# Performance work log

Hardware: AMD Instinct MI355X
Metric: run time of the kernel (lower is better)

The kernel has to match this reference:

```python
import jax, jax.numpy as jnp
import numpy as np

B, S, D_IN, D_OUT, R = 4, 1024, 1024, 1024, 8

def setup_inputs() -> dict:
    key = jax.random.key(0)
    k1, k2, k3, k4, k5 = jax.random.split(key, 5)
    scale = 1.0 / np.sqrt(D_IN)
    return {
        "x": jax.random.normal(k1, (B, S, D_IN), dtype=jnp.float32),
        "A_params": jax.random.normal(k2, (B, S, D_OUT, R), dtype=jnp.float32) * 0.02,
        "B_params": jax.random.normal(k3, (B, S, R, D_IN), dtype=jnp.float32) * 0.02,
        "W": jax.random.normal(k4, (D_OUT, D_IN), dtype=jnp.float32) * scale,
        "b": jax.random.normal(k5, (D_OUT,), dtype=jnp.float32) * scale,
    }

def reference(x, A_params, B_params, W, b):
    # base linear: y = x @ W^T + b  -> [B, S, D_OUT]
    base_out = jnp.einsum('bsi,oi->bso', x, W) + b
    # per-token low-rank update: (x @ B^T) @ A^T
    inter = jnp.einsum('bsi,bsri->bsr', x, B_params)           # [B, S, R]
    adaptation = jnp.einsum('bsr,bsor->bso', inter, A_params)  # [B, S, D_OUT]
    return base_out + adaptation
```

## Files before the change

kernel.cpp:

```cpp
#include <hip/hip_runtime.h>
#include <hip/hip_bf16.h>
#include <stdint.h>

#define TOKENS 4096
#define DIN 1024
#define DOUT 1024
#define RANK 8
#define BM 128
#define BN 64
#define BK 64

typedef __attribute__((ext_vector_type(4))) float f32x4;
typedef __attribute__((ext_vector_type(8))) short short8;

__device__ __forceinline__ unsigned short f2bf(float f) {
    union { float f; unsigned u; } v; v.f = f;
    unsigned r = v.u + 0x7FFFu + ((v.u >> 16) & 1u);
    return (unsigned short)(r >> 16);
}

__global__ __launch_bounds__(256) void k_inter_cvt(const float* __restrict__ x,
                                                   const float* __restrict__ Bp,
                                                   const float* __restrict__ W,
                                                   float* __restrict__ inter,
                                                   ushort* __restrict__ xb,
                                                   ushort* __restrict__ Wb) {
    const int bid = blockIdx.x;
    const int tid = threadIdx.x;

    if (bid >= 1024) {
        const int b2 = bid - 1024;
        const float4* w4 = (const float4*)(W + (size_t)b2 * 4096);
        ushort4* o4 = (ushort4*)(Wb + (size_t)b2 * 4096);
#pragma unroll
        for (int j = 0; j < 4; ++j) {
            float4 v = w4[j * 256 + tid];
            ushort4 u;
            u.x = f2bf(v.x); u.y = f2bf(v.y); u.z = f2bf(v.z); u.w = f2bf(v.w);
            o4[j * 256 + tid] = u;
        }
        return;
    }

    const int lane = tid & 63, wave = tid >> 6;
    const int t = bid * 4 + wave;

    const float4* x4 = (const float4*)(x + (size_t)t * DIN);
    float4 xv[4];
#pragma unroll
    for (int j = 0; j < 4; ++j) xv[j] = x4[j * 64 + lane];

    ushort4* xb4 = (ushort4*)(xb + (size_t)t * DIN);
#pragma unroll
    for (int j = 0; j < 4; ++j) {
        ushort4 u;
        u.x = f2bf(xv[j].x); u.y = f2bf(xv[j].y);
        u.z = f2bf(xv[j].z); u.w = f2bf(xv[j].w);
        xb4[j * 64 + lane] = u;
    }

    const float4* B4 = (const float4*)(Bp + (size_t)t * RANK * DIN);
    float acc[RANK];
#pragma unroll
    for (int r = 0; r < RANK; ++r) {
        float s = 0.f;
#pragma unroll
        for (int j = 0; j < 4; ++j) {
            float4 bv = B4[r * 256 + j * 64 + lane];
            s += bv.x * xv[j].x + bv.y * xv[j].y + bv.z * xv[j].z + bv.w * xv[j].w;
        }
        acc[r] = s;
    }

#pragma unroll
    for (int r = 0; r < RANK; ++r) {
#pragma unroll
        for (int off = 32; off > 0; off >>= 1)
            acc[r] += __shfl_xor(acc[r], off, 64);
    }

    if (lane == 0) {
        float4 lo, hi;
        lo.x = acc[0]; lo.y = acc[1]; lo.z = acc[2]; lo.w = acc[3];
        hi.x = acc[4]; hi.y = acc[5]; hi.z = acc[6]; hi.w = acc[7];
        float4* ip = (float4*)(inter + (size_t)t * RANK);
        ip[0] = lo; ip[1] = hi;
    }
}

__global__ __launch_bounds__(256, 2) void k_gemm_fused(const ushort* __restrict__ Xb,
                                                       const ushort* __restrict__ Wb,
                                                       const float* __restrict__ bias,
                                                       const float* __restrict__ inter,
                                                       const float* __restrict__ Ap,
                                                       float* __restrict__ out) {
    __shared__ ushort As[2][BM * BK];
    __shared__ ushort Bs[2][BN * BK];
    __shared__ float sInter[BM * 8];
    __shared__ float sBias[BN];

    const int tid = threadIdx.x;
    const int lane = tid & 63, wave = tid >> 6;
    const int wm = wave >> 1, wn = wave & 1;

    const int bid = blockIdx.x;
    const int swz = (bid & 7) * 64 + (bid >> 3);
    const int M0 = (swz >> 4) * BM;
    const int N0 = (swz & 15) * BN;

    const int col16 = lane & 15;
    const int kg = lane >> 4;
    const int c8 = col16 & 7;

    ((float4*)sInter)[tid] = ((const float4*)(inter + (size_t)M0 * RANK))[tid];
    if (tid < 16) ((float4*)sBias)[tid] = ((const float4*)(bias + N0))[tid];

    const float* Abase = Ap + ((size_t)(M0 + wm * 64 + kg * 4) * DOUT +
                               (N0 + wn * 32 + col16)) * RANK;

    auto stage = [&](int b, int kt) {
#pragma unroll
        for (int st = 0; st < 4; ++st) {
            int flat = st * 256 + tid;
            int row = flat >> 3, ch = flat & 7;
            int chs = ch ^ (row & 7);
            const ushort* g = Xb + (size_t)(M0 + row) * DIN + kt + chs * 8;
            __builtin_amdgcn_global_load_lds(
                (const __attribute__((address_space(1))) void*)g,
                (__attribute__((address_space(3))) void*)(&As[b][flat * 8]), 16, 0, 0);
        }
#pragma unroll
        for (int st = 0; st < 2; ++st) {
            int flat = st * 256 + tid;
            int row = flat >> 3, ch = flat & 7;
            int chs = ch ^ (row & 7);
            const ushort* g = Wb + (size_t)(N0 + row) * DIN + kt + chs * 8;
            __builtin_amdgcn_global_load_lds(
                (const __attribute__((address_space(1))) void*)g,
                (__attribute__((address_space(3))) void*)(&Bs[b][flat * 8]), 16, 0, 0);
        }
    };

    auto aptr = [&](int e) {
        const int nf = e >> 3, mf = (e >> 1) & 3, rg0 = (e & 1) * 2;
        return Abase + ((size_t)(mf * 16 + rg0) * DOUT + nf * 16) * RANK;
    };

    float4 areg[2][4];

    {
        const float* Ae0 = aptr(0);
        areg[0][0] = ((const float4*)Ae0)[0];
        areg[0][1] = ((const float4*)Ae0)[1];
        areg[0][2] = ((const float4*)(Ae0 + (size_t)DOUT * RANK))[0];
        areg[0][3] = ((const float4*)(Ae0 + (size_t)DOUT * RANK))[1];
    }
    __builtin_amdgcn_sched_barrier(0);
    stage(0, 0);

    f32x4 acc[4][2] = {};

#pragma unroll
    for (int t = 0; t < 16; ++t) {
        const int cur = t & 1;

        if (t < 15) {
            const float* Ae0 = aptr(t + 1);
            areg[cur ^ 1][0] = ((const float4*)Ae0)[0];
            areg[cur ^ 1][1] = ((const float4*)Ae0)[1];
            areg[cur ^ 1][2] = ((const float4*)(Ae0 + (size_t)DOUT * RANK))[0];
            areg[cur ^ 1][3] = ((const float4*)(Ae0 + (size_t)DOUT * RANK))[1];
            __builtin_amdgcn_sched_barrier(0);
            stage(cur ^ 1, (t + 1) * BK);
        }

        if (t == 0) {
            asm volatile("s_waitcnt vmcnt(10) lgkmcnt(0)" ::: "memory");
        } else if (t < 15) {
            asm volatile("s_waitcnt vmcnt(10)" ::: "memory");
        } else {
            asm volatile("s_waitcnt vmcnt(0)" ::: "memory");
        }
        __builtin_amdgcn_s_barrier();

#pragma unroll
        for (int ks = 0; ks < 2; ++ks) {
            short8 a[4], b[2];
#pragma unroll
            for (int m4 = 0; m4 < 4; ++m4) {
                const int chs = (ks * 4 + kg) ^ c8;
                a[m4] = *(const short8*)(&As[cur][(wm * 64 + m4 * 16 + col16) * BK + chs * 8]);
            }
#pragma unroll
            for (int n2 = 0; n2 < 2; ++n2) {
                const int chs = (ks * 4 + kg) ^ c8;
                b[n2] = *(const short8*)(&Bs[cur][(wn * 32 + n2 * 16 + col16) * BK + chs * 8]);
            }
#pragma unroll
            for (int m4 = 0; m4 < 4; ++m4)
#pragma unroll
                for (int n2 = 0; n2 < 2; ++n2)
                    acc[m4][n2] = __builtin_amdgcn_mfma_f32_16x16x32_bf16(
                        a[m4], b[n2], acc[m4][n2], 0, 0, 0);
        }

        {
            const int nf = t >> 3, mf = (t >> 1) & 3, rg0 = (t & 1) * 2;
            const int mloc0 = wm * 64 + mf * 16 + kg * 4 + rg0;
            const float4* iv0 = (const float4*)(sInter + mloc0 * 8);
            const float4* iv1 = (const float4*)(sInter + (mloc0 + 1) * 8);
            float4 i00 = iv0[0], i01 = iv0[1], i10 = iv1[0], i11 = iv1[1];
            float4 a00 = areg[cur][0], a01 = areg[cur][1];
            float4 a10 = areg[cur][2], a11 = areg[cur][3];
            float d0 = a00.x * i00.x + a00.y * i00.y + a00.z * i00.z + a00.w * i00.w +
                       a01.x * i01.x + a01.y * i01.y + a01.z * i01.z + a01.w * i01.w;
            float d1 = a10.x * i10.x + a10.y * i10.y + a10.z * i10.z + a10.w * i10.w +
                       a11.x * i11.x + a11.y * i11.y + a11.z * i11.z + a11.w * i11.w;
            acc[mf][nf][rg0] += d0;
            acc[mf][nf][rg0 + 1] += d1;
        }

        __builtin_amdgcn_s_barrier();
    }

#pragma unroll
    for (int nf = 0; nf < 2; ++nf) {
        const int oc = wn * 32 + nf * 16 + col16;
        const int o = N0 + oc;
        const float bb = sBias[oc];
#pragma unroll
        for (int mf = 0; mf < 4; ++mf) {
#pragma unroll
            for (int rg = 0; rg < 4; ++rg) {
                const int m = M0 + wm * 64 + mf * 16 + kg * 4 + rg;
                out[(size_t)m * DOUT + o] = acc[mf][nf][rg] + bb;
            }
        }
    }
}

extern "C" void kernel_launch(void* const* d_in, const int* in_sizes, int n_in,
                              void* d_out, int out_size, void* d_ws, size_t ws_size,
                              hipStream_t stream) {
    const float* x    = (const float*)d_in[0];
    const float* Ap   = (const float*)d_in[1];
    const float* Bp   = (const float*)d_in[2];
    const float* W    = (const float*)d_in[3];
    const float* bias = (const float*)d_in[4];
    float* out = (float*)d_out;

    ushort* xb = (ushort*)d_ws;
    ushort* Wb = xb + (size_t)TOKENS * DIN;
    float* inter = (float*)(Wb + (size_t)DOUT * DIN);

    hipLaunchKernelGGL(k_inter_cvt, dim3(1024 + 256), dim3(256), 0, stream,
                       x, Bp, W, inter, xb, Wb);
    hipLaunchKernelGGL(k_gemm_fused, dim3((TOKENS / BM) * (DOUT / BN)), dim3(256), 0, stream,
                       xb, Wb, bias, inter, Ap, out);
}
```

Before: 70.20 us.

## Stream B_params and x through LDS with double-buffered async loads in inter kernel

The first kernel now stages B_params and x into shared memory with global_load_lds direct-to-LDS copies. Each block processes four tokens in eight half-rank steps, prefetching the next step into a second buffer while computing the current one. Each wave computes one rank dot product per step instead of eight per token, and writes the bf16 copy of x from LDS. This aims to keep more memory requests in flight for the dominant B_params read (128MB), at the cost of full waitcnt(0) plus a barrier at every step and 40KB of LDS per block, which lowers occupancy.

```diff
diff --git a/kernel.cpp b/kernel.cpp
--- a/kernel.cpp
+++ b/kernel.cpp
@@ -9,6 +9,8 @@
 #define BM 128
 #define BN 64
 #define BK 64
+#define TPB 4
+#define NBI (TOKENS / TPB)
 
 typedef __attribute__((ext_vector_type(4))) float f32x4;
 typedef __attribute__((ext_vector_type(8))) short short8;
@@ -17,6 +19,10 @@
     union { float f; unsigned u; } v; v.f = f;
     unsigned r = v.u + 0x7FFFu + ((v.u >> 16) & 1u);
     return (unsigned short)(r >> 16);
+}
+
+__device__ __forceinline__ float dot4(float4 a, float4 b) {
+    return a.x * b.x + a.y * b.y + a.z * b.z + a.w * b.w;
 }
 
 __global__ __launch_bounds__(256) void k_inter_cvt(const float* __restrict__ x,
@@ -28,8 +34,8 @@
     const int bid = blockIdx.x;
     const int tid = threadIdx.x;
 
-    if (bid >= 1024) {
-        const int b2 = bid - 1024;
+    if (bid >= NBI) {
+        const int b2 = bid - NBI;
         const float4* w4 = (const float4*)(W + (size_t)b2 * 4096);
         ushort4* o4 = (ushort4*)(Wb + (size_t)b2 * 4096);
 #pragma unroll
@@ -42,49 +48,66 @@
         return;
     }
 
-    const int lane = tid & 63, wave = tid >> 6;
-    const int t = bid * 4 + wave;
-
-    const float4* x4 = (const float4*)(x + (size_t)t * DIN);
-    float4 xv[4];
-#pragma unroll
-    for (int j = 0; j < 4; ++j) xv[j] = x4[j * 64 + lane];
-
-    ushort4* xb4 = (ushort4*)(xb + (size_t)t * DIN);
-#pragma unroll
-    for (int j = 0; j < 4; ++j) {
-        ushort4 u;
-        u.x = f2bf(xv[j].x); u.y = f2bf(xv[j].y);
-        u.z = f2bf(xv[j].z); u.w = f2bf(xv[j].w);
-        xb4[j * 64 + lane] = u;
-    }
-
-    const float4* B4 = (const float4*)(Bp + (size_t)t * RANK * DIN);
-    float acc[RANK];
-#pragma unroll
-    for (int r = 0; r < RANK; ++r) {
+    __shared__ float bls[2][4 * 1024];
+    __shared__ float xls[2][1024];
+
+    const int lane = tid & 63, wid = tid >> 6;
+    const int T0 = bid * TPB;
+
+    auto stageB = [&](int buf, int t, int h) {
+#pragma unroll
+        for (int s = 0; s < 4; ++s) {
+            const float* g = Bp + ((size_t)t * RANK + h * 4) * DIN + s * 1024 + tid * 4;
+            __builtin_amdgcn_global_load_lds(
+                (const __attribute__((address_space(1))) void*)g,
+                (__attribute__((address_space(3))) void*)(&bls[buf][s * 1024 + tid * 4]),
+                16, 0, 0);
+        }
+    };
+    auto stageX = [&](int buf, int t) {
+        const float* g = x + (size_t)t * DIN + tid * 4;
+        __builtin_amdgcn_global_load_lds(
+            (const __attribute__((address_space(1))) void*)g,
+            (__attribute__((address_space(3))) void*)(&xls[buf][tid * 4]), 16, 0, 0);
+    };
+
+    stageX(0, T0);
+    stageB(0, T0, 0);
+
+#pragma unroll
+    for (int q = 0; q < 2 * TPB; ++q) {
+        const int tl = q >> 1, h = q & 1;
+        const int t = T0 + tl;
+        const int bb = q & 1, xbuf = tl & 1;
+
+        if (q + 1 < 2 * TPB) stageB((q + 1) & 1, T0 + ((q + 1) >> 1), (q + 1) & 1);
+        if (h == 1 && tl + 1 < TPB) stageX((tl + 1) & 1, t + 1);
+
+        asm volatile("s_waitcnt vmcnt(0)" ::: "memory");
+        __builtin_amdgcn_s_barrier();
+
+        const float* br = &bls[bb][wid * 1024];
+        const float* xr = &xls[xbuf][0];
         float s = 0.f;
 #pragma unroll
         for (int j = 0; j < 4; ++j) {
-            float4 bv = B4[r * 256 + j * 64 + lane];
-            s += bv.x * xv[j].x + bv.y * xv[j].y + bv.z * xv[j].z + bv.w * xv[j].w;
-        }
-        acc[r] = s;
-    }
-
-#pragma unroll
-    for (int r = 0; r < RANK; ++r) {
+            float4 bv = *(const float4*)(br + j * 256 + lane * 4);
+            float4 xv = *(const float4*)(xr + j * 256 + lane * 4);
+            s += dot4(bv, xv);
+        }
 #pragma unroll
         for (int off = 32; off > 0; off >>= 1)
-            acc[r] += __shfl_xor(acc[r], off, 64);
-    }
-
-    if (lane == 0) {
-        float4 lo, hi;
-        lo.x = acc[0]; lo.y = acc[1]; lo.z = acc[2]; lo.w = acc[3];
-        hi.x = acc[4]; hi.y = acc[5]; hi.z = acc[6]; hi.w = acc[7];
-        float4* ip = (float4*)(inter + (size_t)t * RANK);
-        ip[0] = lo; ip[1] = hi;
+            s += __shfl_xor(s, off, 64);
+        if (lane == 0) inter[(size_t)t * RANK + h * 4 + wid] = s;
+
+        if (h == 0) {
+            float4 v = *(const float4*)(xr + wid * 256 + lane * 4);
+            ushort4 u;
+            u.x = f2bf(v.x); u.y = f2bf(v.y); u.z = f2bf(v.z); u.w = f2bf(v.w);
+            *(ushort4*)(xb + (size_t)t * DIN + wid * 256 + lane * 4) = u;
+        }
+
+        __builtin_amdgcn_s_barrier();
     }
 }
 
@@ -212,10 +235,8 @@
             float4 i00 = iv0[0], i01 = iv0[1], i10 = iv1[0], i11 = iv1[1];
             float4 a00 = areg[cur][0], a01 = areg[cur][1];
             float4 a10 = areg[cur][2], a11 = areg[cur][3];
-            float d0 = a00.x * i00.x + a00.y * i00.y + a00.z * i00.z + a00.w * i00.w +
-                       a01.x * i01.x + a01.y * i01.y + a01.z * i01.z + a01.w * i01.w;
-            float d1 = a10.x * i10.x + a10.y * i10.y + a10.z * i10.z + a10.w * i10.w +
-                       a11.x * i11.x + a11.y * i11.y + a11.z * i11.z + a11.w * i11.w;
+            float d0 = dot4(a00, i00) + dot4(a01, i01);
+            float d1 = dot4(a10, i10) + dot4(a11, i11);
             acc[mf][nf][rg0] += d0;
             acc[mf][nf][rg0 + 1] += d1;
         }
@@ -253,7 +274,7 @@
     ushort* Wb = xb + (size_t)TOKENS * DIN;
     float* inter = (float*)(Wb + (size_t)DOUT * DIN);
 
-    hipLaunchKernelGGL(k_inter_cvt, dim3(1024 + 256), dim3(256), 0, stream,
+    hipLaunchKernelGGL(k_inter_cvt, dim3(NBI + 256), dim3(256), 0, stream,
                        x, Bp, W, inter, xb, Wb);
     hipLaunchKernelGGL(k_gemm_fused, dim3((TOKENS / BM) * (DOUT / BN)), dim3(256), 0, stream,
                        xb, Wb, bias, inter, Ap, out);
```

After: 71.04 us. About the same (+1.2%).
